# Performance work log

Measured on AMD Instinct MI355X. Metric: run time of the kernel, lower is better.

Reference implementation:

```python
import jax, jax.numpy as jnp
import numpy as np

N_NODES = 100000
N_EDGES = 1600000
IN_CH = 128
HID = 128
OUT_CH = 10


def setup_inputs() -> dict:
    key = jax.random.key(0)
    ks = jax.random.split(key, 14)
    s_in = 1.0 / np.sqrt(IN_CH)
    s_h = 1.0 / np.sqrt(HID)
    return {
        "x0": jax.random.normal(ks[0], (N_NODES, IN_CH), jnp.float32),
        "edge_index": jax.random.randint(ks[1], (2, N_EDGES), 0, N_NODES, jnp.int32),
        "edge_weight": jax.random.uniform(ks[2], (N_EDGES,), jnp.float32),
        # GraphConv layer 1 (in -> hid): lin_rel (weight+bias) applied to aggregated msgs, lin_root (no bias)
        "W1_rel": jax.random.uniform(ks[3], (IN_CH, HID), jnp.float32, -s_in, s_in),
        "b1": jax.random.uniform(ks[4], (HID,), jnp.float32, -s_in, s_in),
        "W1_root": jax.random.uniform(ks[5], (IN_CH, HID), jnp.float32, -s_in, s_in),
        # GraphConv layer 2 (hid -> hid)
        "W2_rel": jax.random.uniform(ks[6], (HID, HID), jnp.float32, -s_h, s_h),
        "b2": jax.random.uniform(ks[7], (HID,), jnp.float32, -s_h, s_h),
        "W2_root": jax.random.uniform(ks[8], (HID, HID), jnp.float32, -s_h, s_h),
        # GraphConv layer 3 (hid -> hid)
        "W3_rel": jax.random.uniform(ks[9], (HID, HID), jnp.float32, -s_h, s_h),
        "b3": jax.random.uniform(ks[10], (HID,), jnp.float32, -s_h, s_h),
        "W3_root": jax.random.uniform(ks[11], (HID, HID), jnp.float32, -s_h, s_h),
        # classification head
        "W_lin": jax.random.uniform(ks[12], (HID, OUT_CH), jnp.float32, -s_h, s_h),
        "b_lin": jax.random.uniform(ks[13], (OUT_CH,), jnp.float32, -s_h, s_h),
    }


def _graph_conv(x, src, dst, ew, W_rel, b_rel, W_root):
    # message: x_j * w_e ; aggregate: scatter-add onto dst ; update: lin_rel(agg) + lin_root(x)
    msg = x[src] * ew[:, None]                                   # [E, C]
    agg = jax.ops.segment_sum(msg, dst, num_segments=x.shape[0])  # [N, C]
    return agg @ W_rel + b_rel + x @ W_root                      # [N, C']


def reference(x0, edge_index, edge_weight,
              W1_rel, b1, W1_root,
              W2_rel, b2, W2_root,
              W3_rel, b3, W3_root,
              W_lin, b_lin):
    src, dst = edge_index[0], edge_index[1]
    # dropout p=0.2 is identity in eval mode
    x1 = jax.nn.relu(_graph_conv(x0, src, dst, edge_weight, W1_rel, b1, W1_root))
    x2 = jax.nn.relu(_graph_conv(x1, src, dst, edge_weight, W2_rel, b2, W2_root))
    x3 = jax.nn.relu(_graph_conv(x2, src, dst, edge_weight, W3_rel, b3, W3_root))
    logits = x3 @ W_lin + b_lin
    return jax.nn.log_softmax(logits, axis=-1)
```

## Files before the change

### kernel.cpp

```cpp
#include <hip/hip_runtime.h>
#include <hip/hip_bf16.h>
#include <math.h>

#define C128 128
#define OUT_CH 10

typedef __attribute__((ext_vector_type(8))) short short8;
typedef __attribute__((ext_vector_type(4))) float f32x4;
typedef __attribute__((ext_vector_type(2))) float f32x2;
typedef __attribute__((ext_vector_type(4))) int i32x4;

__device__ __forceinline__ unsigned short f2bf(float f) {
    unsigned b = __float_as_uint(f);
    unsigned r = (b + 0x7FFF + ((b >> 16) & 1)) >> 16;
    return (unsigned short)r;
}
__device__ __forceinline__ float bf2f(unsigned short u) {
    return __uint_as_float(((unsigned)u) << 16);
}


#define NBMAX 400
#define BCAP  4608
#define P1K   4096

__global__ __launch_bounds__(512) void bin_kernel(
    const int* __restrict__ ei, const float* __restrict__ ew,
    int* __restrict__ gcur, unsigned* __restrict__ bins_rec,
    unsigned char* __restrict__ bins_dst, int E, int nb)
{
    __shared__ int cnt[NBMAX];
    __shared__ int pos[NBMAX];
    __shared__ int gbase[NBMAX];
    __shared__ int s[512];
    __shared__ int totalSh;
    __shared__ uint2 buf[P1K];

    const int t = threadIdx.x;
    const int e0 = blockIdx.x * P1K;

    for (int b = t; b < nb; b += 512) { cnt[b] = 0; pos[b] = 0; }
    __syncthreads();

    unsigned rec[8];
    int dstv[8];
    const int e = e0 + t * 8;
    if (e + 8 <= E) {
        i32x4 d0 = __builtin_nontemporal_load((const i32x4*)(ei + E + e));
        i32x4 d1 = __builtin_nontemporal_load((const i32x4*)(ei + E + e + 4));
        i32x4 s0 = __builtin_nontemporal_load((const i32x4*)(ei + e));
        i32x4 s1 = __builtin_nontemporal_load((const i32x4*)(ei + e + 4));
        f32x4 w0 = __builtin_nontemporal_load((const f32x4*)(ew + e));
        f32x4 w1 = __builtin_nontemporal_load((const f32x4*)(ew + e + 4));
        int dd[8] = {d0.x, d0.y, d0.z, d0.w, d1.x, d1.y, d1.z, d1.w};
        int ss[8] = {s0.x, s0.y, s0.z, s0.w, s1.x, s1.y, s1.z, s1.w};
        float ww[8] = {w0.x, w0.y, w0.z, w0.w, w1.x, w1.y, w1.z, w1.w};
#pragma unroll
        for (int j = 0; j < 8; ++j) {
            unsigned wb = __float_as_uint(ww[j]);
            unsigned r  = ((wb + 0x7FFF + ((wb >> 16) & 1)) >> 16) & 0x7FFFu;
            rec[j]  = (unsigned)ss[j] | (r << 17);
            dstv[j] = dd[j];
            atomicAdd(&cnt[dd[j] >> 8], 1);
        }
    } else {
#pragma unroll
        for (int j = 0; j < 8; ++j) {
            int ee = e + j;
            if (ee < E) {
                int dst = ei[E + ee];
                unsigned wb = __float_as_uint(ew[ee]);
                unsigned r  = ((wb + 0x7FFF + ((wb >> 16) & 1)) >> 16) & 0x7FFFu;
                rec[j]  = (unsigned)ei[ee] | (r << 17);
                dstv[j] = dst;
                atomicAdd(&cnt[dst >> 8], 1);
            } else {
                dstv[j] = -1;
            }
        }
    }
    __syncthreads();

    int c = (t < nb) ? cnt[t] : 0;
    s[t] = c;
    __syncthreads();
    for (int o = 1; o < 512; o <<= 1) {
        int u = (t >= o) ? s[t - o] : 0;
        __syncthreads();
        s[t] += u;
        __syncthreads();
    }
    if (t == nb - 1) totalSh = s[t];
    __syncthreads();

#pragma unroll
    for (int j = 0; j < 8; ++j) {
        if (dstv[j] >= 0) {
            int b = dstv[j] >> 8;
            int r = atomicAdd(&pos[b], 1);
            buf[s[b] - cnt[b] + r] = make_uint2(rec[j], (unsigned)dstv[j]);
        }
    }
    __syncthreads();

    if (t < nb) {
        int b = t + (int)((blockIdx.x * 131u) % (unsigned)nb);
        if (b >= nb) b -= nb;
        int cb = cnt[b];
        if (cb > 0) gbase[b] = atomicAdd(&gcur[b], cb);
    }
    __syncthreads();

    const int total = totalSh;
    for (int i = t; i < total; i += 512) {
        uint2 v = buf[i];
        int b = (int)(v.y >> 8);
        int dest = gbase[b] + (i - (s[b] - cnt[b]));
        if (dest < BCAP) {
            bins_rec[(size_t)b * BCAP + dest] = v.x;
            bins_dst[(size_t)b * BCAP + dest] = (unsigned char)(v.y & 255u);
        }
    }
}

__global__ __launch_bounds__(512) void bucket_scan_kernel(
    const int* __restrict__ gcur, int* __restrict__ bbase,
    int* __restrict__ row_ptr, int nb, int N, int E)
{
    __shared__ int s[512];
    int t = threadIdx.x;
    int v = (t < nb) ? gcur[t] : 0;
    s[t] = v;
    __syncthreads();
    for (int o = 1; o < 512; o <<= 1) {
        int u = (t >= o) ? s[t - o] : 0;
        __syncthreads();
        s[t] += u;
        __syncthreads();
    }
    if (t < nb) bbase[t] = s[t] - v;
    if (t == 0) row_ptr[N] = E;
}

__global__ __launch_bounds__(256) void build_kernel(
    const unsigned* __restrict__ bins_rec, const unsigned char* __restrict__ bins_dst,
    const int* __restrict__ gcur, const int* __restrict__ bbase,
    int* __restrict__ row_ptr, unsigned* __restrict__ csr, int N)
{
    __shared__ int rowCnt[256];
    __shared__ int rowOff[256];
    __shared__ int sc[256];
    __shared__ unsigned out[BCAP];

    const int b = blockIdx.x, t = threadIdx.x;
    int cnt = gcur[b];
    if (cnt > BCAP) cnt = BCAP;
    const int base = bbase[b];
    const unsigned* mbr = bins_rec + (size_t)b * BCAP;
    const unsigned char* mbd = bins_dst + (size_t)b * BCAP;

    rowCnt[t] = 0;
    __syncthreads();
    for (int i = t; i < cnt; i += 256) atomicAdd(&rowCnt[(int)mbd[i]], 1);
    __syncthreads();

    int v = rowCnt[t];
    sc[t] = v;
    __syncthreads();
    for (int o = 1; o < 256; o <<= 1) {
        int u = (t >= o) ? sc[t - o] : 0;
        __syncthreads();
        sc[t] += u;
        __syncthreads();
    }
    rowOff[t] = sc[t] - v;
    int idx = b * 256 + t;
    if (idx <= N) row_ptr[idx] = base + sc[t] - v;
    rowCnt[t] = 0;
    __syncthreads();

    for (int i = t; i < cnt; i += 256) {
        int d = (int)mbd[i];
        int k = atomicAdd(&rowCnt[d], 1);
        out[rowOff[d] + k] = mbr[i];
    }
    __syncthreads();

    for (int i = t; i < cnt; i += 256) csr[base + i] = out[i];
}


__global__ __launch_bounds__(256) void cvt_both_kernel(const float4* __restrict__ x,
                                                       ushort4* __restrict__ xb,
                                                       unsigned* __restrict__ xf8, int n4) {
    int i = blockIdx.x * blockDim.x + threadIdx.x;
    if (i < n4) {
        float4 v = x[i];
        ushort4 o;
        o.x = f2bf(v.x); o.y = f2bf(v.y); o.z = f2bf(v.z); o.w = f2bf(v.w);
        xb[i] = o;
        unsigned p = __builtin_amdgcn_cvt_pk_fp8_f32(v.x, v.y, 0, false);
        p = __builtin_amdgcn_cvt_pk_fp8_f32(v.z, v.w, p, true);
        xf8[i] = p;
    }
}


__global__ __launch_bounds__(256) void pack_all_kernel(
    const float* __restrict__ W1r, const float* __restrict__ W1t,
    const float* __restrict__ W2r, const float* __restrict__ W2t,
    const float* __restrict__ W3r, const float* __restrict__ W3t,
    const float* __restrict__ Wl,
    unsigned short* __restrict__ Wp1, unsigned short* __restrict__ Wp2,
    unsigned short* __restrict__ Wp3, unsigned short* __restrict__ WlP)
{
    int b = blockIdx.x;
    if (b < 384) {
        int which = b >> 7;
        const float* Wr = (which == 0) ? W1r : (which == 1) ? W2r : W3r;
        const float* Wt = (which == 0) ? W1t : (which == 1) ? W2t : W3t;
        unsigned short* Wp = (which == 0) ? Wp1 : (which == 1) ? Wp2 : Wp3;
        int idx = (b & 127) * 256 + threadIdx.x;
        int j    = idx & 7;
        int n    = (idx >> 3) & 127;
        int quad = (idx >> 10) & 3;
        int ks   = idx >> 12;
        const float* W = (ks < 4) ? Wr : Wt;
        int k = (ks & 3) * 32 + quad * 8 + j;
        Wp[idx] = f2bf(W[(size_t)k * C128 + n]);
    } else {
        int idx = (b - 384) * 256 + threadIdx.x;
        int j    = idx & 7;
        int col  = (idx >> 3) & 15;
        int quad = (idx >> 7) & 3;
        int ks   = (idx >> 9) & 3;
        int half = idx >> 11;
        int k = ks * 32 + quad * 8 + j;
        float v = (col < OUT_CH) ? Wl[(size_t)k * OUT_CH + col] : 0.f;
        unsigned short hi = f2bf(v);
        unsigned short outv = hi;
        if (half) outv = f2bf(v - bf2f(hi));
        WlP[idx] = outv;
    }
}


#define AGS 136

#define GATHER_BODY(rec_, rem_, acc2_)                                          \
    for (int c = 0; c < (rem_); c += 16) {                                      \
        int i0e = c + g, i1e = c + 4 + g, i2e = c + 8 + g, i3e = c + 12 + g;    \
        int s0 = __shfl((rec_), i0e & 63, 64);                                  \
        int s1 = __shfl((rec_), i1e & 63, 64);                                  \
        int s2 = __shfl((rec_), i2e & 63, 64);                                  \
        int s3 = __shfl((rec_), i3e & 63, 64);                                  \
        float w0 = (i0e < (rem_)) ? __uint_as_float(((unsigned)s0 >> 17) << 16) : 0.f; \
        float w1 = (i1e < (rem_)) ? __uint_as_float(((unsigned)s1 >> 17) << 16) : 0.f; \
        float w2 = (i2e < (rem_)) ? __uint_as_float(((unsigned)s2 >> 17) << 16) : 0.f; \
        float w3 = (i3e < (rem_)) ? __uint_as_float(((unsigned)s3 >> 17) << 16) : 0.f; \
        uint2 q0 = *(const uint2*)&xf8[(unsigned)(s0 & 0x1FFFF) * 32u + l16 * 2]; \
        uint2 q1 = *(const uint2*)&xf8[(unsigned)(s1 & 0x1FFFF) * 32u + l16 * 2]; \
        uint2 q2 = *(const uint2*)&xf8[(unsigned)(s2 & 0x1FFFF) * 32u + l16 * 2]; \
        uint2 q3 = *(const uint2*)&xf8[(unsigned)(s3 & 0x1FFFF) * 32u + l16 * 2]; \
        { f32x2 w2v = {w0, w0};                                                 \
          (acc2_)[0] += __builtin_amdgcn_cvt_pk_f32_fp8(q0.x, false) * w2v;     \
          (acc2_)[1] += __builtin_amdgcn_cvt_pk_f32_fp8(q0.x, true)  * w2v;     \
          (acc2_)[2] += __builtin_amdgcn_cvt_pk_f32_fp8(q0.y, false) * w2v;     \
          (acc2_)[3] += __builtin_amdgcn_cvt_pk_f32_fp8(q0.y, true)  * w2v; }   \
        { f32x2 w2v = {w1, w1};                                                 \
          (acc2_)[0] += __builtin_amdgcn_cvt_pk_f32_fp8(q1.x, false) * w2v;     \
          (acc2_)[1] += __builtin_amdgcn_cvt_pk_f32_fp8(q1.x, true)  * w2v;     \
          (acc2_)[2] += __builtin_amdgcn_cvt_pk_f32_fp8(q1.y, false) * w2v;     \
          (acc2_)[3] += __builtin_amdgcn_cvt_pk_f32_fp8(q1.y, true)  * w2v; }   \
        { f32x2 w2v = {w2, w2};                                                 \
          (acc2_)[0] += __builtin_amdgcn_cvt_pk_f32_fp8(q2.x, false) * w2v;     \
          (acc2_)[1] += __builtin_amdgcn_cvt_pk_f32_fp8(q2.x, true)  * w2v;     \
          (acc2_)[2] += __builtin_amdgcn_cvt_pk_f32_fp8(q2.y, false) * w2v;     \
          (acc2_)[3] += __builtin_amdgcn_cvt_pk_f32_fp8(q2.y, true)  * w2v; }   \
        { f32x2 w2v = {w3, w3};                                                 \
          (acc2_)[0] += __builtin_amdgcn_cvt_pk_f32_fp8(q3.x, false) * w2v;     \
          (acc2_)[1] += __builtin_amdgcn_cvt_pk_f32_fp8(q3.x, true)  * w2v;     \
          (acc2_)[2] += __builtin_amdgcn_cvt_pk_f32_fp8(q3.y, false) * w2v;     \
          (acc2_)[3] += __builtin_amdgcn_cvt_pk_f32_fp8(q3.y, true)  * w2v; }   \
    }

#define GATHER_PHASE                                                            \
                                     \
    if (w < 4) {                                                                \
        int rrow = tile0 + w * 4 + g;                                           \
        int srow = (rrow < N) ? rrow : 0;                                       \
        uint4 v = *(const uint4*)&xb[(size_t)srow * C128 + l16 * 8];            \
        *(uint4*)&XR[(w * 4 + g) * AGS + l16 * 8] = v;                          \
    }                                                                           \
                    \
    int pi0[2], pdeg[2], prec[2];                                               \
    _Pragma("unroll")                                                           \
    for (int i = 0; i < 2; ++i) {                                               \
        int node = tile0 + w * 2 + i;                                           \
        int a = 0, d = 0;                                                       \
        if (node < N) { a = row_ptr[node]; d = row_ptr[node + 1] - a; }         \
        pi0[i] = a; pdeg[i] = d;                                                \
    }                                                                           \
    _Pragma("unroll")                                                           \
    for (int i = 0; i < 2; ++i) {                                               \
        prec[i] = 0;                                                            \
        if (lane < pdeg[i])                                                     \
            prec[i] = (int)__builtin_nontemporal_load(&csr[pi0[i] + lane]);     \
    }                                                                           \
    _Pragma("unroll")                                                           \
    for (int i = 0; i < 2; ++i) {                                               \
        int deg = pdeg[i];                                                      \
        f32x2 acc2[4];                                                          \
        acc2[0] = acc2[1] = acc2[2] = acc2[3] = (f32x2){0.f, 0.f};              \
        int rem0 = (deg < 64) ? deg : 64;                                       \
        GATHER_BODY(prec[i], rem0, acc2)                                        \
        for (int base = 64; base < deg; base += 64) {                           \
            int rem = deg - base; if (rem > 64) rem = 64;                       \
            int rec = 0;                                                        \
            if (base + lane < deg)                                              \
                rec = (int)__builtin_nontemporal_load(&csr[pi0[i] + base + lane]); \
            GATHER_BODY(rec, rem, acc2)                                         \
        }                                                                       \
        _Pragma("unroll")                                                       \
        for (int j = 0; j < 4; ++j) {                                           \
            acc2[j].x += __shfl_xor(acc2[j].x, 16, 64);                         \
            acc2[j].y += __shfl_xor(acc2[j].y, 16, 64);                         \
            acc2[j].x += __shfl_xor(acc2[j].x, 32, 64);                         \
            acc2[j].y += __shfl_xor(acc2[j].y, 32, 64);                         \
        }                                                                       \
        if (g == 0) {                                                           \
            uint4 o;                                                            \
            o.x = (unsigned)f2bf(acc2[0].x) | ((unsigned)f2bf(acc2[0].y) << 16); \
            o.y = (unsigned)f2bf(acc2[1].x) | ((unsigned)f2bf(acc2[1].y) << 16); \
            o.z = (unsigned)f2bf(acc2[2].x) | ((unsigned)f2bf(acc2[2].y) << 16); \
            o.w = (unsigned)f2bf(acc2[3].x) | ((unsigned)f2bf(acc2[3].y) << 16); \
            *(uint4*)&AG[(w * 2 + i) * AGS + l16 * 8] = o;                      \
        }                                                                       \
    }

__global__ __launch_bounds__(512) void fused_layer(
    const unsigned* __restrict__ xf8,
    const int* __restrict__ row_ptr,
    const unsigned* __restrict__ csr,
    const unsigned short* __restrict__ xb,
    const unsigned short* __restrict__ Wp,
    const float* __restrict__ bias,
    unsigned short* __restrict__ outb, unsigned char* __restrict__ outf8, int N)
{
    __shared__ unsigned short AG[16 * AGS];
    __shared__ unsigned short XR[16 * AGS];

    const int t = threadIdx.x;
    const int w    = t >> 6;
    const int lane = t & 63;
    const int l16  = lane & 15;
    const int g    = lane >> 4;
    const int tile0 = blockIdx.x * 16;

    GATHER_PHASE
    __syncthreads();

    const int l15 = l16, quad = g;
    const int nt = w;
    float bv = bias[nt * 16 + l15];
    f32x4 acc = (f32x4){0.f, 0.f, 0.f, 0.f};

#pragma unroll
    for (int ks = 0; ks < 8; ++ks) {
        short8 a;
        if (ks < 4) a = *(const short8*)&AG[l15 * AGS + ks * 32 + quad * 8];
        else        a = *(const short8*)&XR[l15 * AGS + (ks - 4) * 32 + quad * 8];
        short8 b = *(const short8*)&Wp[(((ks * 4 + quad) * 128) + nt * 16 + l15) * 8];
        acc = __builtin_amdgcn_mfma_f32_16x16x32_bf16(a, b, acc, 0, 0, 0);
    }

#pragma unroll
    for (int r = 0; r < 4; ++r) {
        int row = tile0 + quad * 4 + r;
        if (row < N) {
            float v = fmaxf(acc[r] + bv, 0.f);
            outb[(size_t)row * C128 + nt * 16 + l15] = f2bf(v);
            unsigned p8 = __builtin_amdgcn_cvt_pk_fp8_f32(v, 0.f, 0, false);
            outf8[(size_t)row * C128 + nt * 16 + l15] = (unsigned char)(p8 & 0xff);
        }
    }
}

__global__ __launch_bounds__(512) void fused_layer_head(
    const unsigned* __restrict__ xf8,
    const int* __restrict__ row_ptr,
    const unsigned* __restrict__ csr,
    const unsigned short* __restrict__ xb,
    const unsigned short* __restrict__ Wp,
    const float* __restrict__ bias,
    const unsigned short* __restrict__ WlP, const float* __restrict__ bl,
    float* __restrict__ out, int N)
{
    __shared__ unsigned short AG[16 * AGS];
    __shared__ unsigned short XR[16 * AGS];

    const int t = threadIdx.x;
    const int w    = t >> 6;
    const int lane = t & 63;
    const int l16  = lane & 15;
    const int g    = lane >> 4;
    const int tile0 = blockIdx.x * 16;

    GATHER_PHASE
    __syncthreads();

    const int l15 = l16, quad = g;
    const int nt = w;
    float bv = bias[nt * 16 + l15];
    f32x4 acc = (f32x4){0.f, 0.f, 0.f, 0.f};

#pragma unroll
    for (int ks = 0; ks < 8; ++ks) {
        short8 a;
        if (ks < 4) a = *(const short8*)&AG[l15 * AGS + ks * 32 + quad * 8];
        else        a = *(const short8*)&XR[l15 * AGS + (ks - 4) * 32 + quad * 8];
        short8 b = *(const short8*)&Wp[(((ks * 4 + quad) * 128) + nt * 16 + l15) * 8];
        acc = __builtin_amdgcn_mfma_f32_16x16x32_bf16(a, b, acc, 0, 0, 0);
    }

    __syncthreads();
#pragma unroll
    for (int r = 0; r < 4; ++r) {
        int lrow = quad * 4 + r;
        float v = fmaxf(acc[r] + bv, 0.f);
        AG[lrow * AGS + nt * 16 + l15] = f2bf(v);
    }
    __syncthreads();

    if (w == 0) {
        f32x4 hacc = (f32x4){0.f, 0.f, 0.f, 0.f};
#pragma unroll
        for (int ks = 0; ks < 4; ++ks) {
            short8 a2  = *(const short8*)&AG[l15 * AGS + ks * 32 + quad * 8];
            short8 bh  = *(const short8*)&WlP[(((ks * 4 + quad) * 16) + l15) * 8];
            short8 bl2 = *(const short8*)&WlP[2048 + (((ks * 4 + quad) * 16) + l15) * 8];
            hacc = __builtin_amdgcn_mfma_f32_16x16x32_bf16(a2, bh, hacc, 0, 0, 0);
            hacc = __builtin_amdgcn_mfma_f32_16x16x32_bf16(a2, bl2, hacc, 0, 0, 0);
        }
        float blv = (l15 < OUT_CH) ? bl[l15] : 0.f;
#pragma unroll
        for (int r = 0; r < 4; ++r) {
            int row = tile0 + quad * 4 + r;
            float lg = (l15 < OUT_CH) ? (hacc[r] + blv) : -1e30f;
            float m = lg;
            m = fmaxf(m, __shfl_xor(m, 1, 64));
            m = fmaxf(m, __shfl_xor(m, 2, 64));
            m = fmaxf(m, __shfl_xor(m, 4, 64));
            m = fmaxf(m, __shfl_xor(m, 8, 64));
            float s = __expf(lg - m);
            s += __shfl_xor(s, 1, 64);
            s += __shfl_xor(s, 2, 64);
            s += __shfl_xor(s, 4, 64);
            s += __shfl_xor(s, 8, 64);
            float lse = m + __logf(s);
            if (l15 < OUT_CH && row < N)
                out[(size_t)row * OUT_CH + l15] = lg - lse;
        }
    }
}


extern "C" void kernel_launch(void* const* d_in, const int* in_sizes, int n_in,
                              void* d_out, int out_size, void* d_ws, size_t ws_size,
                              hipStream_t stream) {
    const float* x0   = (const float*)d_in[0];
    const int*   ei   = (const int*)  d_in[1];
    const float* ew   = (const float*)d_in[2];
    const float* W1r  = (const float*)d_in[3];
    const float* b1   = (const float*)d_in[4];
    const float* W1t  = (const float*)d_in[5];
    const float* W2r  = (const float*)d_in[6];
    const float* b2   = (const float*)d_in[7];
    const float* W2t  = (const float*)d_in[8];
    const float* W3r  = (const float*)d_in[9];
    const float* b3   = (const float*)d_in[10];
    const float* W3t  = (const float*)d_in[11];
    const float* Wlin = (const float*)d_in[12];
    const float* blin = (const float*)d_in[13];

    const int N = in_sizes[0] / C128;
    const int E = in_sizes[1] / 2;
    const int nb = (N + 255) >> 8;

    char* ws = (char*)d_ws;
    size_t off = 0;
    auto alloc = [&](size_t bytes) {
        void* p = ws + off;
        off = (off + bytes + 255) & ~(size_t)255;
        return p;
    };
    size_t bb = (size_t)N * C128 * sizeof(unsigned short);
    size_t fb = (size_t)N * C128;
    unsigned short* xb0  = (unsigned short*)alloc(bb);
    unsigned short* xb1  = (unsigned short*)alloc(bb);
    unsigned char*  xf8a = (unsigned char*)alloc(fb);
    unsigned char*  xf8b = (unsigned char*)alloc(fb);
    unsigned short* Wp1  = (unsigned short*)alloc(32768 * 2);
    unsigned short* Wp2  = (unsigned short*)alloc(32768 * 2);
    unsigned short* Wp3  = (unsigned short*)alloc(32768 * 2);
    unsigned short* WlP  = (unsigned short*)alloc(4096 * 2);
    unsigned* csr  = (unsigned*)alloc((size_t)E * 4);
    int* row_ptr   = (int*)alloc((size_t)(N + 2) * 4);
    unsigned* bins_rec  = (unsigned*)alloc((size_t)nb * BCAP * 4);
    unsigned char* bins_dst = (unsigned char*)alloc((size_t)nb * BCAP);
    int* gcur      = (int*)alloc((size_t)nb * 4);
    int* bbase     = (int*)alloc((size_t)nb * 4);

    hipMemsetAsync(gcur, 0, (size_t)nb * sizeof(int), stream);
    bin_kernel<<<(E + P1K - 1) / P1K, 512, 0, stream>>>(ei, ew, gcur, bins_rec, bins_dst, E, nb);
    bucket_scan_kernel<<<1, 512, 0, stream>>>(gcur, bbase, row_ptr, nb, N, E);
    build_kernel<<<nb, 256, 0, stream>>>(bins_rec, bins_dst, gcur, bbase, row_ptr, csr, N);

    cvt_both_kernel<<<(N * C128 / 4 + 255) / 256, 256, 0, stream>>>(
        (const float4*)x0, (ushort4*)xb0, (unsigned*)xf8a, N * C128 / 4);
    pack_all_kernel<<<400, 256, 0, stream>>>(W1r, W1t, W2r, W2t, W3r, W3t, Wlin,
                                             Wp1, Wp2, Wp3, WlP);

    const int fusedGrid = (N + 15) / 16;

    fused_layer<<<fusedGrid, 512, 0, stream>>>(
        (const unsigned*)xf8a, row_ptr, csr, xb0, Wp1, b1, xb1, xf8b, N);
    fused_layer<<<fusedGrid, 512, 0, stream>>>(
        (const unsigned*)xf8b, row_ptr, csr, xb1, Wp2, b2, xb0, xf8a, N);
    fused_layer_head<<<fusedGrid, 512, 0, stream>>>(
        (const unsigned*)xf8a, row_ptr, csr, xb0, Wp3, b3, WlP, blin,
        (float*)d_out, N);
}
```

Baseline: 364.4 us.

## Merge binning, input conversion and weight packing into one prep kernel; fold bucket scan into build

The edge binning, the fp32-to-bf16/fp8 conversion of the input and the weight packing now run as different block ranges of a single prep kernel. The separate single-block bucket scan kernel is removed: each build block recomputes the prefix sum over the bucket counts itself to find its base offset. The goal is to cut kernel launches and serialization gaps and to let independent preprocessing overlap. The costs are that the conversion and packing blocks carry the binning kernel's large shared-memory footprint, which can limit occupancy, and that every build block repeats a small redundant scan.

```diff
diff --git a/kernel.cpp b/kernel.cpp
--- a/kernel.cpp
+++ b/kernel.cpp
@@ -24,10 +24,19 @@
 #define BCAP  4608
 #define P1K   4096
 
-__global__ __launch_bounds__(512) void bin_kernel(
+
+__global__ __launch_bounds__(512) void prep_kernel(
     const int* __restrict__ ei, const float* __restrict__ ew,
     int* __restrict__ gcur, unsigned* __restrict__ bins_rec,
-    unsigned char* __restrict__ bins_dst, int E, int nb)
+    unsigned char* __restrict__ bins_dst, int E, int nb, int binBlocks,
+    const float4* __restrict__ x, ushort4* __restrict__ xb,
+    unsigned* __restrict__ xf8, int n4, int cvtBlocks,
+    const float* __restrict__ W1r, const float* __restrict__ W1t,
+    const float* __restrict__ W2r, const float* __restrict__ W2t,
+    const float* __restrict__ W3r, const float* __restrict__ W3t,
+    const float* __restrict__ Wl,
+    unsigned short* __restrict__ Wp1, unsigned short* __restrict__ Wp2,
+    unsigned short* __restrict__ Wp3, unsigned short* __restrict__ WlP)
 {
     __shared__ int cnt[NBMAX];
     __shared__ int pos[NBMAX];
@@ -36,8 +45,56 @@
     __shared__ int totalSh;
     __shared__ uint2 buf[P1K];
 
+    const int blk = blockIdx.x;
     const int t = threadIdx.x;
-    const int e0 = blockIdx.x * P1K;
+
+    if (blk >= binBlocks) {
+        int b2 = blk - binBlocks;
+        if (b2 < cvtBlocks) {
+            int i = b2 * 512 + t;
+            if (i < n4) {
+                float4 v = x[i];
+                ushort4 o;
+                o.x = f2bf(v.x); o.y = f2bf(v.y); o.z = f2bf(v.z); o.w = f2bf(v.w);
+                xb[i] = o;
+                unsigned p = __builtin_amdgcn_cvt_pk_fp8_f32(v.x, v.y, 0, false);
+                p = __builtin_amdgcn_cvt_pk_fp8_f32(v.z, v.w, p, true);
+                xf8[i] = p;
+            }
+        } else {
+            int idx = (b2 - cvtBlocks) * 512 + t;
+            if (idx < 3 * 32768) {
+                int which = idx >> 15;
+                int lx = idx & 32767;
+                const float* Wr = (which == 0) ? W1r : (which == 1) ? W2r : W3r;
+                const float* Wt = (which == 0) ? W1t : (which == 1) ? W2t : W3t;
+                unsigned short* Wp = (which == 0) ? Wp1 : (which == 1) ? Wp2 : Wp3;
+                int j    = lx & 7;
+                int n    = (lx >> 3) & 127;
+                int quad = (lx >> 10) & 3;
+                int ks   = lx >> 12;
+                const float* W = (ks < 4) ? Wr : Wt;
+                int k = (ks & 3) * 32 + quad * 8 + j;
+                Wp[lx] = f2bf(W[(size_t)k * C128 + n]);
+            } else if (idx < 3 * 32768 + 4096) {
+                int lx = idx - 3 * 32768;
+                int j    = lx & 7;
+                int col  = (lx >> 3) & 15;
+                int quad = (lx >> 7) & 3;
+                int ks   = (lx >> 9) & 3;
+                int half = lx >> 11;
+                int k = ks * 32 + quad * 8 + j;
+                float v = (col < OUT_CH) ? Wl[(size_t)k * OUT_CH + col] : 0.f;
+                unsigned short hi = f2bf(v);
+                unsigned short outv = hi;
+                if (half) outv = f2bf(v - bf2f(hi));
+                WlP[lx] = outv;
+            }
+        }
+        return;
+    }
+
+    const int e0 = blk * P1K;
 
     for (int b = t; b < nb; b += 512) { cnt[b] = 0; pos[b] = 0; }
     __syncthreads();
@@ -104,7 +161,7 @@
     __syncthreads();
 
     if (t < nb) {
-        int b = t + (int)((blockIdx.x * 131u) % (unsigned)nb);
+        int b = t + (int)((blk * 131u) % (unsigned)nb);
         if (b >= nb) b -= nb;
         int cb = cnt[b];
         if (cb > 0) gbase[b] = atomicAdd(&gcur[b], cb);
@@ -123,49 +180,23 @@
     }
 }
 
-__global__ __launch_bounds__(512) void bucket_scan_kernel(
-    const int* __restrict__ gcur, int* __restrict__ bbase,
-    int* __restrict__ row_ptr, int nb, int N, int E)
-{
-    __shared__ int s[512];
-    int t = threadIdx.x;
-    int v = (t < nb) ? gcur[t] : 0;
-    s[t] = v;
-    __syncthreads();
-    for (int o = 1; o < 512; o <<= 1) {
-        int u = (t >= o) ? s[t - o] : 0;
-        __syncthreads();
-        s[t] += u;
-        __syncthreads();
-    }
-    if (t < nb) bbase[t] = s[t] - v;
-    if (t == 0) row_ptr[N] = E;
-}
 
 __global__ __launch_bounds__(256) void build_kernel(
     const unsigned* __restrict__ bins_rec, const unsigned char* __restrict__ bins_dst,
-    const int* __restrict__ gcur, const int* __restrict__ bbase,
-    int* __restrict__ row_ptr, unsigned* __restrict__ csr, int N)
+    const int* __restrict__ gcur, int* __restrict__ row_ptr,
+    unsigned* __restrict__ csr, int N, int nb)
 {
     __shared__ int rowCnt[256];
     __shared__ int rowOff[256];
     __shared__ int sc[256];
     __shared__ unsigned out[BCAP];
+    __shared__ int baseSh;
 
     const int b = blockIdx.x, t = threadIdx.x;
-    int cnt = gcur[b];
-    if (cnt > BCAP) cnt = BCAP;
-    const int base = bbase[b];
-    const unsigned* mbr = bins_rec + (size_t)b * BCAP;
-    const unsigned char* mbd = bins_dst + (size_t)b * BCAP;
-
-    rowCnt[t] = 0;
-    __syncthreads();
-    for (int i = t; i < cnt; i += 256) atomicAdd(&rowCnt[(int)mbd[i]], 1);
-    __syncthreads();
-
-    int v = rowCnt[t];
-    sc[t] = v;
+
+    int a0 = (2 * t < nb) ? gcur[2 * t] : 0;
+    int a1 = (2 * t + 1 < nb) ? gcur[2 * t + 1] : 0;
+    sc[t] = a0 + a1;
     __syncthreads();
     for (int o = 1; o < 256; o <<= 1) {
         int u = (t >= o) ? sc[t - o] : 0;
@@ -173,6 +204,32 @@
         sc[t] += u;
         __syncthreads();
     }
+    if (t == (b >> 1)) {
+        int excl = sc[t] - (a0 + a1);
+        baseSh = excl + ((b & 1) ? a0 : 0);
+    }
+    __syncthreads();
+    const int base = baseSh;
+
+    int cnt = gcur[b];
+    if (cnt > BCAP) cnt = BCAP;
+    const unsigned* mbr = bins_rec + (size_t)b * BCAP;
+    const unsigned char* mbd = bins_dst + (size_t)b * BCAP;
+
+    rowCnt[t] = 0;
+    __syncthreads();
+    for (int i = t; i < cnt; i += 256) atomicAdd(&rowCnt[(int)mbd[i]], 1);
+    __syncthreads();
+
+    int v = rowCnt[t];
+    sc[t] = v;
+    __syncthreads();
+    for (int o = 1; o < 256; o <<= 1) {
+        int u = (t >= o) ? sc[t - o] : 0;
+        __syncthreads();
+        sc[t] += u;
+        __syncthreads();
+    }
     rowOff[t] = sc[t] - v;
     int idx = b * 256 + t;
     if (idx <= N) row_ptr[idx] = base + sc[t] - v;
@@ -187,61 +244,6 @@
     __syncthreads();
 
     for (int i = t; i < cnt; i += 256) csr[base + i] = out[i];
-}
-
-
-__global__ __launch_bounds__(256) void cvt_both_kernel(const float4* __restrict__ x,
-                                                       ushort4* __restrict__ xb,
-                                                       unsigned* __restrict__ xf8, int n4) {
-    int i = blockIdx.x * blockDim.x + threadIdx.x;
-    if (i < n4) {
-        float4 v = x[i];
-        ushort4 o;
-        o.x = f2bf(v.x); o.y = f2bf(v.y); o.z = f2bf(v.z); o.w = f2bf(v.w);
-        xb[i] = o;
-        unsigned p = __builtin_amdgcn_cvt_pk_fp8_f32(v.x, v.y, 0, false);
-        p = __builtin_amdgcn_cvt_pk_fp8_f32(v.z, v.w, p, true);
-        xf8[i] = p;
-    }
-}
-
-
-__global__ __launch_bounds__(256) void pack_all_kernel(
-    const float* __restrict__ W1r, const float* __restrict__ W1t,
-    const float* __restrict__ W2r, const float* __restrict__ W2t,
-    const float* __restrict__ W3r, const float* __restrict__ W3t,
-    const float* __restrict__ Wl,
-    unsigned short* __restrict__ Wp1, unsigned short* __restrict__ Wp2,
-    unsigned short* __restrict__ Wp3, unsigned short* __restrict__ WlP)
-{
-    int b = blockIdx.x;
-    if (b < 384) {
-        int which = b >> 7;
-        const float* Wr = (which == 0) ? W1r : (which == 1) ? W2r : W3r;
-        const float* Wt = (which == 0) ? W1t : (which == 1) ? W2t : W3t;
-        unsigned short* Wp = (which == 0) ? Wp1 : (which == 1) ? Wp2 : Wp3;
-        int idx = (b & 127) * 256 + threadIdx.x;
-        int j    = idx & 7;
-        int n    = (idx >> 3) & 127;
-        int quad = (idx >> 10) & 3;
-        int ks   = idx >> 12;
-        const float* W = (ks < 4) ? Wr : Wt;
-        int k = (ks & 3) * 32 + quad * 8 + j;
-        Wp[idx] = f2bf(W[(size_t)k * C128 + n]);
-    } else {
-        int idx = (b - 384) * 256 + threadIdx.x;
-        int j    = idx & 7;
-        int col  = (idx >> 3) & 15;
-        int quad = (idx >> 7) & 3;
-        int ks   = (idx >> 9) & 3;
-        int half = idx >> 11;
-        int k = ks * 32 + quad * 8 + j;
-        float v = (col < OUT_CH) ? Wl[(size_t)k * OUT_CH + col] : 0.f;
-        unsigned short hi = f2bf(v);
-        unsigned short outv = hi;
-        if (half) outv = f2bf(v - bf2f(hi));
-        WlP[idx] = outv;
-    }
 }
 
 
@@ -285,14 +287,12 @@
     }
 
 #define GATHER_PHASE                                                            \
-                                     \
     if (w < 4) {                                                                \
         int rrow = tile0 + w * 4 + g;                                           \
         int srow = (rrow < N) ? rrow : 0;                                       \
         uint4 v = *(const uint4*)&xb[(size_t)srow * C128 + l16 * 8];            \
         *(uint4*)&XR[(w * 4 + g) * AGS + l16 * 8] = v;                          \
     }                                                                           \
-                    \
     int pi0[2], pdeg[2], prec[2];                                               \
     _Pragma("unroll")                                                           \
     for (int i = 0; i < 2; ++i) {                                               \
@@ -486,6 +486,7 @@
     const int N = in_sizes[0] / C128;
     const int E = in_sizes[1] / 2;
     const int nb = (N + 255) >> 8;
+    const int n4 = N * C128 / 4;
 
     char* ws = (char*)d_ws;
     size_t off = 0;
@@ -509,17 +510,19 @@
     unsigned* bins_rec  = (unsigned*)alloc((size_t)nb * BCAP * 4);
     unsigned char* bins_dst = (unsigned char*)alloc((size_t)nb * BCAP);
     int* gcur      = (int*)alloc((size_t)nb * 4);
-    int* bbase     = (int*)alloc((size_t)nb * 4);
+
+    const int binBlocks = (E + P1K - 1) / P1K;
+    const int cvtBlocks = (n4 + 511) / 512;
+    const int packBlocks = (3 * 32768 + 4096 + 511) / 512;
+    const int prepGrid = binBlocks + cvtBlocks + packBlocks;
 
     hipMemsetAsync(gcur, 0, (size_t)nb * sizeof(int), stream);
-    bin_kernel<<<(E + P1K - 1) / P1K, 512, 0, stream>>>(ei, ew, gcur, bins_rec, bins_dst, E, nb);
-    bucket_scan_kernel<<<1, 512, 0, stream>>>(gcur, bbase, row_ptr, nb, N, E);
-    build_kernel<<<nb, 256, 0, stream>>>(bins_rec, bins_dst, gcur, bbase, row_ptr, csr, N);
-
-    cvt_both_kernel<<<(N * C128 / 4 + 255) / 256, 256, 0, stream>>>(
-        (const float4*)x0, (ushort4*)xb0, (unsigned*)xf8a, N * C128 / 4);
-    pack_all_kernel<<<400, 256, 0, stream>>>(W1r, W1t, W2r, W2t, W3r, W3t, Wlin,
-                                             Wp1, Wp2, Wp3, WlP);
+    prep_kernel<<<prepGrid, 512, 0, stream>>>(
+        ei, ew, gcur, bins_rec, bins_dst, E, nb, binBlocks,
+        (const float4*)x0, (ushort4*)xb0, (unsigned*)xf8a, n4, cvtBlocks,
+        W1r, W1t, W2r, W2t, W3r, W3t, Wlin, Wp1, Wp2, Wp3, WlP);
+
+    build_kernel<<<nb, 256, 0, stream>>>(bins_rec, bins_dst, gcur, row_ptr, csr, N, nb);
 
     const int fusedGrid = (N + 15) / 16;
 
```

Measured after the change: 353.9 us. -2.9%, faster.
